# Optimization experiments

Hardware: AMD Instinct MI355X
Metric: run time of the kernel (lower is better)

## Reference

```python
import jax, jax.numpy as jnp
import numpy as np

# BCQLinear packed forward: weight[o, i] reconstructed from per-(out,group,bit)
# alpha scales and +/-1 binary codes via einsum('oib,oiab->oia'), then a plain
# out-channel-wise matmul (in_ch_wise=False) plus bias. beta is NOT used in the
# packed forward path of the original module.

B, S = 2, 1024          # token dims (m...)
O = 4096                 # out_features
G, A, NB = 32, 128, 3    # n_groups, group_size, n_bits; in_features = G*A = 4096


def setup_inputs() -> dict:
    key = jax.random.key(0)
    k1, k2, k3, k4 = jax.random.split(key, 4)
    x = jax.random.normal(k1, (B, S, G * A), dtype=jnp.float32)
    # binary codes are strictly +/-1 (Packer.unpack yields sign bits)
    b = jnp.sign(jax.random.normal(k2, (O, G, A, NB)))
    binary = jnp.where(b == 0, 1.0, b).astype(jnp.float32)
    # alpha scales are small positive magnitudes in practice
    alpha = jax.random.uniform(k3, (O, G, NB), dtype=jnp.float32,
                               minval=0.01, maxval=0.1)
    bias = 0.01 * jax.random.normal(k4, (O,), dtype=jnp.float32)
    return {"input": x, "binary": binary, "alpha": alpha, "bias": bias}


def reference(input, binary, alpha, bias):
    # dequantize: [O, G, A] -> [O, I]
    weight = jnp.einsum('oib,oiab->oia', alpha, binary).reshape(binary.shape[0], -1)
    # out-channel-wise matmul: m...i, oi -> m...o
    out = jnp.einsum('msi,oi->mso', input, weight) + bias
    return out
```

## Files before the change

### kernel.cpp

```cpp
#include <hip/hip_runtime.h>
#include <hip/hip_bf16.h>
#include <stdint.h>

typedef __bf16 bf16x8 __attribute__((ext_vector_type(8)));
typedef __bf16 bf16x4 __attribute__((ext_vector_type(4)));
typedef float  f32x4  __attribute__((ext_vector_type(4)));

static constexpr int Mdim = 2048;
static constexpr int Ndim = 4096;
static constexpr int Kdim = 4096;
static constexpr int DQ_BLOCKS = (Ndim * Kdim / 4) / 256;
static constexpr int CVT_BLOCKS = (Mdim * Kdim / 8) / 256;

__global__ __launch_bounds__(256)
void prep(const float* __restrict__ binary, const float* __restrict__ alpha,
          const float* __restrict__ x, __bf16* __restrict__ w,
          __bf16* __restrict__ xb) {
  const int b = blockIdx.x;
  if (b < DQ_BLOCKS) {
    long e = ((long)b * 256 + threadIdx.x) * 4;
    int o = (int)(e >> 12);
    int i = (int)(e & 4095);
    int g = i >> 7;
    const float* al = alpha + ((long)o * 32 + g) * 3;
    float a0 = al[0], a1 = al[1], a2 = al[2];
    const float4* bs = (const float4*)(binary + e * 3);
    float4 b0 = bs[0], b1 = bs[1], b2 = bs[2];
    bf16x4 wv;
    wv[0] = (__bf16)(a0 * b0.x + a1 * b0.y + a2 * b0.z);
    wv[1] = (__bf16)(a0 * b0.w + a1 * b1.x + a2 * b1.y);
    wv[2] = (__bf16)(a0 * b1.z + a1 * b1.w + a2 * b2.x);
    wv[3] = (__bf16)(a0 * b2.y + a1 * b2.z + a2 * b2.w);
    *(bf16x4*)(w + e) = wv;
  } else {
    long e = ((long)(b - DQ_BLOCKS) * 256 + threadIdx.x) * 8;
    float4 v0 = *(const float4*)(x + e);
    float4 v1 = *(const float4*)(x + e + 4);
    bf16x8 r;
    r[0] = (__bf16)v0.x; r[1] = (__bf16)v0.y; r[2] = (__bf16)v0.z; r[3] = (__bf16)v0.w;
    r[4] = (__bf16)v1.x; r[5] = (__bf16)v1.y; r[6] = (__bf16)v1.z; r[7] = (__bf16)v1.w;
    *(bf16x8*)(xb + e) = r;
  }
}

__global__ __launch_bounds__(256)
void reduce_add(const __bf16* __restrict__ p, const float* __restrict__ bias,
                float* __restrict__ out) {
  long e = ((long)blockIdx.x * 256 + threadIdx.x) * 8;
  bf16x8 a = *(const bf16x8*)(p + e);
  bf16x8 c = *(const bf16x8*)(p + (long)Mdim * Ndim + e);
  int col = (int)(e & (Ndim - 1));
  float4 bv0 = *(const float4*)(bias + col);
  float4 bv1 = *(const float4*)(bias + col + 4);
  float4 r0, r1;
  r0.x = (float)a[0] + (float)c[0] + bv0.x;
  r0.y = (float)a[1] + (float)c[1] + bv0.y;
  r0.z = (float)a[2] + (float)c[2] + bv0.z;
  r0.w = (float)a[3] + (float)c[3] + bv0.w;
  r1.x = (float)a[4] + (float)c[4] + bv1.x;
  r1.y = (float)a[5] + (float)c[5] + bv1.y;
  r1.z = (float)a[6] + (float)c[6] + bv1.z;
  r1.w = (float)a[7] + (float)c[7] + bv1.w;
  *(float4*)(out + e) = r0;
  *(float4*)(out + e + 4) = r1;
}

static constexpr int BK = 64;
static constexpr int KSLICE = 2048;
static constexpr int NT = KSLICE / BK;
static constexpr int ITERS = NT / 2;

__device__ __forceinline__ void g2l16(const void* g, void* l) {
  __builtin_amdgcn_global_load_lds(
      (const __attribute__((address_space(1))) void*)g,
      (__attribute__((address_space(3))) void*)l, 16, 0, 0);
}

#define BAR()    __builtin_amdgcn_s_barrier()
#define LGKM0()  asm volatile("s_waitcnt lgkmcnt(0)" ::: "memory")
#define SCHED0() __builtin_amdgcn_sched_barrier(0)

#define STAGE_A(t, H, b) do { \
  _Pragma("unroll") for (int j_ = 0; j_ < 2; ++j_) \
    g2l16(baseA[j_] + (H) * 128 * Kdim + (t) * 64, \
          sm + (b) * 65536 + (H) * 16384 + (w * 2 + j_) * 1024); \
} while (0)
#define STAGE_B(t, H, b) do { \
  _Pragma("unroll") for (int j_ = 0; j_ < 2; ++j_) \
    g2l16(baseB[j_] + (H) * 128 * Kdim + (t) * 64, \
          sm + (b) * 65536 + 32768 + (H) * 16384 + (w * 2 + j_) * 1024); \
} while (0)

#define LOAD_A4(dst, b, m0_) do { \
  _Pragma("unroll") for (int m_ = 0; m_ < 4; ++m_) \
    _Pragma("unroll") for (int h_ = 0; h_ < 2; ++h_) \
      dst[m_][h_] = *(const bf16x8*)(sm + (b) * 65536 + aoffbase + ((m0_) + m_) * 2048 + swz[h_]); \
} while (0)
#define LOAD_B2(dst, b, n0_) do { \
  _Pragma("unroll") for (int n_ = 0; n_ < 2; ++n_) \
    _Pragma("unroll") for (int h_ = 0; h_ < 2; ++h_) \
      dst[n_][h_] = *(const bf16x8*)(sm + (b) * 65536 + boffbase + ((n0_) + n_) * 2048 + swz[h_]); \
} while (0)

#define MMA8(fa_, fb_, m0_, n0_) do { \
  __builtin_amdgcn_s_setprio(1); \
  _Pragma("unroll") for (int m_ = 0; m_ < 4; ++m_) \
    _Pragma("unroll") for (int n_ = 0; n_ < 2; ++n_) { \
      acc[(m0_) + m_][(n0_) + n_] = __builtin_amdgcn_mfma_f32_16x16x32_bf16( \
          fa_[m_][0], fb_[n_][0], acc[(m0_) + m_][(n0_) + n_], 0, 0, 0); \
      acc[(m0_) + m_][(n0_) + n_] = __builtin_amdgcn_mfma_f32_16x16x32_bf16( \
          fa_[m_][1], fb_[n_][1], acc[(m0_) + m_][(n0_) + n_], 0, 0, 0); \
    } \
  __builtin_amdgcn_s_setprio(0); \
} while (0)

__global__ __launch_bounds__(512, 2)
void gemm8(const __bf16* __restrict__ A, const __bf16* __restrict__ Bw,
           __bf16* __restrict__ P) {
  __shared__ __align__(128) char sm[131072];
  const int tid = threadIdx.x, lane = tid & 63, w = tid >> 6;
  const int wm = w >> 2, wn = w & 3;

  const int bid = blockIdx.x;
  const int logical = (bid & 7) * 32 + (bid >> 3);
  const int ks = logical >> 7;
  const int tile = logical & 127;
  const int tm = tile & 7, tn = tile >> 3;
  const int kbase = ks * KSLICE;

  __bf16* Pout = P + (long)ks * Mdim * Ndim;

  const int rlo = lane >> 3;
  const int gsw = (lane & 7) ^ rlo;
  const __bf16* baseA[2];
  const __bf16* baseB[2];
#pragma unroll
  for (int j = 0; j < 2; ++j) {
    int rp = (w * 2 + j) * 8 + rlo;
    baseA[j] = A  + (long)(tm * 256 + rp) * Kdim + kbase + gsw * 8;
    baseB[j] = Bw + (long)(tn * 256 + rp) * Kdim + kbase + gsw * 8;
  }

  int swz[2];
#pragma unroll
  for (int h = 0; h < 2; ++h)
    swz[h] = (((h * 4 + (lane >> 4)) ^ (lane & 7)) << 4);
  const int aoffbase = (wm * 128 + (lane & 15)) * 128;
  const int boffbase = 32768 + (wn * 64 + (lane & 15)) * 128;

  f32x4 acc[8][4] = {};

  STAGE_A(0, 0, 0); STAGE_A(0, 1, 0); STAGE_B(0, 0, 0); STAGE_B(0, 1, 0);
  STAGE_B(1, 0, 1); STAGE_B(1, 1, 1);
  asm volatile("s_waitcnt vmcnt(4)" ::: "memory");
  BAR();

  bf16x8 fa[4][2], fb01[2][2], fb23[2][2];

  for (int i = 0; i < ITERS; ++i) {
    const int t0 = 2 * i, t1 = 2 * i + 1;
    const bool pf = (i < ITERS - 1);
    LOAD_A4(fa, 0, 0); LOAD_B2(fb01, 0, 0);
    STAGE_A(t1, 0, 1);
    BAR(); LGKM0(); SCHED0();
    MMA8(fa, fb01, 0, 0);
    BAR();
    LOAD_B2(fb23, 0, 2);
    STAGE_A(t1, 1, 1);
    BAR(); LGKM0(); SCHED0();
    MMA8(fa, fb23, 0, 2);
    BAR();
    LOAD_A4(fa, 0, 4);
    if (pf) STAGE_B(t0 + 2, 0, 0);
    BAR(); LGKM0(); SCHED0();
    MMA8(fa, fb01, 4, 0);
    BAR();
    if (pf) STAGE_B(t0 + 2, 1, 0);
    if (i == ITERS - 1) { asm volatile("s_waitcnt vmcnt(0)" ::: "memory"); }
    else                { asm volatile("s_waitcnt vmcnt(4)" ::: "memory"); }
    BAR();
    MMA8(fa, fb23, 4, 2);
    BAR();
    LOAD_A4(fa, 1, 0); LOAD_B2(fb01, 1, 0);
    if (pf) STAGE_A(t0 + 2, 0, 0);
    BAR(); LGKM0(); SCHED0();
    MMA8(fa, fb01, 0, 0);
    BAR();
    LOAD_B2(fb23, 1, 2);
    if (pf) STAGE_A(t0 + 2, 1, 0);
    BAR(); LGKM0(); SCHED0();
    MMA8(fa, fb23, 0, 2);
    BAR();
    LOAD_A4(fa, 1, 4);
    if (pf) STAGE_B(t1 + 2, 0, 1);
    BAR(); LGKM0(); SCHED0();
    MMA8(fa, fb01, 4, 0);
    BAR();
    if (pf) STAGE_B(t1 + 2, 1, 1);
    asm volatile("s_waitcnt vmcnt(4)" ::: "memory");
    BAR();
    MMA8(fa, fb23, 4, 2);
    BAR();
  }

  const int r4 = (lane >> 4) * 4;
  const int cl = lane & 15;
#pragma unroll
  for (int m = 0; m < 8; ++m)
#pragma unroll
    for (int n = 0; n < 4; ++n)
#pragma unroll
      for (int r = 0; r < 4; ++r) {
        int row = tm * 256 + wm * 128 + m * 16 + r4 + r;
        int col = tn * 256 + wn * 64 + n * 16 + cl;
        Pout[(long)row * Ndim + col] = (__bf16)acc[m][n][r];
      }
}

extern "C" void kernel_launch(void* const* d_in, const int* in_sizes, int n_in,
                              void* d_out, int out_size, void* d_ws, size_t ws_size,
                              hipStream_t stream) {
  const float* x      = (const float*)d_in[0];
  const float* binary = (const float*)d_in[1];
  const float* alpha  = (const float*)d_in[2];
  const float* bias   = (const float*)d_in[3];
  float* out = (float*)d_out;

  __bf16* wb = (__bf16*)d_ws;
  __bf16* xb = wb + (size_t)Ndim * Kdim;
  __bf16* pp = xb + (size_t)Mdim * Kdim;

  prep<<<dim3(DQ_BLOCKS + CVT_BLOCKS), 256, 0, stream>>>(binary, alpha, x, wb, xb);
  gemm8<<<dim3(256), 512, 0, stream>>>(xb, wb, pp);
  reduce_add<<<dim3(Mdim * Ndim / 8 / 256), 256, 0, stream>>>(pp, bias, out);
}
```

Baseline: 123.3 us.

## Replace split-K GEMM and reduce kernel with full-K 256x128 tiles and fused bias

Drops the split-K decomposition and its separate reduce_add kernel. Each of the 256 blocks now computes a 256x128 output tile over the full K range and writes fp32 output with the bias added directly. It switches to a three-stage LDS ring buffer (48KB per stage) with a deeper prefetch distance. This removes the bf16 partial-sum round trip and one kernel launch, and avoids the rounding of partials to bf16. In exchange, each block runs twice as many K iterations and the tile has a lower compute-to-load ratio, so B is reloaded more often.

```diff
diff --git a/kernel.cpp b/kernel.cpp
--- a/kernel.cpp
+++ b/kernel.cpp
@@ -43,32 +43,8 @@
   }
 }
 
-__global__ __launch_bounds__(256)
-void reduce_add(const __bf16* __restrict__ p, const float* __restrict__ bias,
-                float* __restrict__ out) {
-  long e = ((long)blockIdx.x * 256 + threadIdx.x) * 8;
-  bf16x8 a = *(const bf16x8*)(p + e);
-  bf16x8 c = *(const bf16x8*)(p + (long)Mdim * Ndim + e);
-  int col = (int)(e & (Ndim - 1));
-  float4 bv0 = *(const float4*)(bias + col);
-  float4 bv1 = *(const float4*)(bias + col + 4);
-  float4 r0, r1;
-  r0.x = (float)a[0] + (float)c[0] + bv0.x;
-  r0.y = (float)a[1] + (float)c[1] + bv0.y;
-  r0.z = (float)a[2] + (float)c[2] + bv0.z;
-  r0.w = (float)a[3] + (float)c[3] + bv0.w;
-  r1.x = (float)a[4] + (float)c[4] + bv1.x;
-  r1.y = (float)a[5] + (float)c[5] + bv1.y;
-  r1.z = (float)a[6] + (float)c[6] + bv1.z;
-  r1.w = (float)a[7] + (float)c[7] + bv1.w;
-  *(float4*)(out + e) = r0;
-  *(float4*)(out + e + 4) = r1;
-}
-
-static constexpr int BK = 64;
-static constexpr int KSLICE = 2048;
-static constexpr int NT = KSLICE / BK;
-static constexpr int ITERS = NT / 2;
+static constexpr int NT = Kdim / 64;
+static constexpr int BUF = 49152;
 
 __device__ __forceinline__ void g2l16(const void* g, void* l) {
   __builtin_amdgcn_global_load_lds(
@@ -79,56 +55,54 @@
 #define BAR()    __builtin_amdgcn_s_barrier()
 #define LGKM0()  asm volatile("s_waitcnt lgkmcnt(0)" ::: "memory")
 #define SCHED0() __builtin_amdgcn_sched_barrier(0)
+#define VMC6()   asm volatile("s_waitcnt vmcnt(6)" ::: "memory")
+#define VMC0()   asm volatile("s_waitcnt vmcnt(0)" ::: "memory")
 
-#define STAGE_A(t, H, b) do { \
+#define STAGE_A(t, H, bo) do { \
   _Pragma("unroll") for (int j_ = 0; j_ < 2; ++j_) \
-    g2l16(baseA[j_] + (H) * 128 * Kdim + (t) * 64, \
-          sm + (b) * 65536 + (H) * 16384 + (w * 2 + j_) * 1024); \
+    g2l16(baseA[j_] + (H) * 128 * (long)Kdim + (t) * 64, \
+          sm + (bo) + (H) * 16384 + (w * 2 + j_) * 1024); \
 } while (0)
-#define STAGE_B(t, H, b) do { \
+#define STAGE_B(t, bo) do { \
   _Pragma("unroll") for (int j_ = 0; j_ < 2; ++j_) \
-    g2l16(baseB[j_] + (H) * 128 * Kdim + (t) * 64, \
-          sm + (b) * 65536 + 32768 + (H) * 16384 + (w * 2 + j_) * 1024); \
+    g2l16(baseB[j_] + (t) * 64, \
+          sm + (bo) + 32768 + (w * 2 + j_) * 1024); \
 } while (0)
 
-#define LOAD_A4(dst, b, m0_) do { \
+#define LOAD_A4(dst, bo, m0_) do { \
   _Pragma("unroll") for (int m_ = 0; m_ < 4; ++m_) \
     _Pragma("unroll") for (int h_ = 0; h_ < 2; ++h_) \
-      dst[m_][h_] = *(const bf16x8*)(sm + (b) * 65536 + aoffbase + ((m0_) + m_) * 2048 + swz[h_]); \
+      dst[m_][h_] = *(const bf16x8*)(sm + (bo) + aoffbase + ((m0_) + m_) * 2048 + swz[h_]); \
 } while (0)
-#define LOAD_B2(dst, b, n0_) do { \
+#define LOAD_B2(dst, bo) do { \
   _Pragma("unroll") for (int n_ = 0; n_ < 2; ++n_) \
     _Pragma("unroll") for (int h_ = 0; h_ < 2; ++h_) \
-      dst[n_][h_] = *(const bf16x8*)(sm + (b) * 65536 + boffbase + ((n0_) + n_) * 2048 + swz[h_]); \
+      dst[n_][h_] = *(const bf16x8*)(sm + (bo) + boffbase + n_ * 2048 + swz[h_]); \
 } while (0)
 
-#define MMA8(fa_, fb_, m0_, n0_) do { \
+#define MMA16(fa_, fb_, m0_) do { \
   __builtin_amdgcn_s_setprio(1); \
   _Pragma("unroll") for (int m_ = 0; m_ < 4; ++m_) \
     _Pragma("unroll") for (int n_ = 0; n_ < 2; ++n_) { \
-      acc[(m0_) + m_][(n0_) + n_] = __builtin_amdgcn_mfma_f32_16x16x32_bf16( \
-          fa_[m_][0], fb_[n_][0], acc[(m0_) + m_][(n0_) + n_], 0, 0, 0); \
-      acc[(m0_) + m_][(n0_) + n_] = __builtin_amdgcn_mfma_f32_16x16x32_bf16( \
-          fa_[m_][1], fb_[n_][1], acc[(m0_) + m_][(n0_) + n_], 0, 0, 0); \
+      acc[(m0_) + m_][n_] = __builtin_amdgcn_mfma_f32_16x16x32_bf16( \
+          fa_[m_][0], fb_[n_][0], acc[(m0_) + m_][n_], 0, 0, 0); \
+      acc[(m0_) + m_][n_] = __builtin_amdgcn_mfma_f32_16x16x32_bf16( \
+          fa_[m_][1], fb_[n_][1], acc[(m0_) + m_][n_], 0, 0, 0); \
     } \
   __builtin_amdgcn_s_setprio(0); \
 } while (0)
 
 __global__ __launch_bounds__(512, 2)
-void gemm8(const __bf16* __restrict__ A, const __bf16* __restrict__ Bw,
-           __bf16* __restrict__ P) {
-  __shared__ __align__(128) char sm[131072];
+void gemm3(const __bf16* __restrict__ A, const __bf16* __restrict__ Bw,
+           const float* __restrict__ bias, float* __restrict__ out) {
+  __shared__ __align__(128) char sm[3 * BUF];
   const int tid = threadIdx.x, lane = tid & 63, w = tid >> 6;
   const int wm = w >> 2, wn = w & 3;
 
   const int bid = blockIdx.x;
   const int logical = (bid & 7) * 32 + (bid >> 3);
-  const int ks = logical >> 7;
-  const int tile = logical & 127;
-  const int tm = tile & 7, tn = tile >> 3;
-  const int kbase = ks * KSLICE;
-
-  __bf16* Pout = P + (long)ks * Mdim * Ndim;
+  const int tm = logical & 7;
+  const int tn = logical >> 3;
 
   const int rlo = lane >> 3;
   const int gsw = (lane & 7) ^ rlo;
@@ -137,8 +111,8 @@
 #pragma unroll
   for (int j = 0; j < 2; ++j) {
     int rp = (w * 2 + j) * 8 + rlo;
-    baseA[j] = A  + (long)(tm * 256 + rp) * Kdim + kbase + gsw * 8;
-    baseB[j] = Bw + (long)(tn * 256 + rp) * Kdim + kbase + gsw * 8;
+    baseA[j] = A  + (long)(tm * 256 + rp) * Kdim + gsw * 8;
+    baseB[j] = Bw + (long)(tn * 128 + rp) * Kdim + gsw * 8;
   }
 
   int swz[2];
@@ -146,75 +120,49 @@
   for (int h = 0; h < 2; ++h)
     swz[h] = (((h * 4 + (lane >> 4)) ^ (lane & 7)) << 4);
   const int aoffbase = (wm * 128 + (lane & 15)) * 128;
-  const int boffbase = 32768 + (wn * 64 + (lane & 15)) * 128;
+  const int boffbase = 32768 + (wn * 32 + (lane & 15)) * 128;
 
-  f32x4 acc[8][4] = {};
+  f32x4 acc[8][2] = {};
 
-  STAGE_A(0, 0, 0); STAGE_A(0, 1, 0); STAGE_B(0, 0, 0); STAGE_B(0, 1, 0);
-  STAGE_B(1, 0, 1); STAGE_B(1, 1, 1);
-  asm volatile("s_waitcnt vmcnt(4)" ::: "memory");
+  STAGE_A(0, 0, 0);     STAGE_A(0, 1, 0);     STAGE_B(0, 0);
+  STAGE_A(1, 0, BUF);   STAGE_A(1, 1, BUF);   STAGE_B(1, BUF);
+  VMC6();
   BAR();
 
-  bf16x8 fa[4][2], fb01[2][2], fb23[2][2];
+  bf16x8 fa[4][2], fa2[4][2], fb[2][2];
+  int ba = 0, bb = BUF, bc = 2 * BUF;
 
-  for (int i = 0; i < ITERS; ++i) {
-    const int t0 = 2 * i, t1 = 2 * i + 1;
-    const bool pf = (i < ITERS - 1);
-    LOAD_A4(fa, 0, 0); LOAD_B2(fb01, 0, 0);
-    STAGE_A(t1, 0, 1);
+  for (int t = 0; t < NT; ++t) {
+    const bool pf = (t + 2 < NT);
+    LOAD_A4(fa, ba, 0);
+    LOAD_B2(fb, ba);
+    if (pf) STAGE_A(t + 2, 0, bc);
     BAR(); LGKM0(); SCHED0();
-    MMA8(fa, fb01, 0, 0);
+    MMA16(fa, fb, 0);
     BAR();
-    LOAD_B2(fb23, 0, 2);
-    STAGE_A(t1, 1, 1);
+    LOAD_A4(fa2, ba, 4);
+    if (pf) { STAGE_A(t + 2, 1, bc); STAGE_B(t + 2, bc); }
+    if (t < NT - 2) { VMC6(); } else { VMC0(); }
     BAR(); LGKM0(); SCHED0();
-    MMA8(fa, fb23, 0, 2);
+    MMA16(fa2, fb, 4);
     BAR();
-    LOAD_A4(fa, 0, 4);
-    if (pf) STAGE_B(t0 + 2, 0, 0);
-    BAR(); LGKM0(); SCHED0();
-    MMA8(fa, fb01, 4, 0);
-    BAR();
-    if (pf) STAGE_B(t0 + 2, 1, 0);
-    if (i == ITERS - 1) { asm volatile("s_waitcnt vmcnt(0)" ::: "memory"); }
-    else                { asm volatile("s_waitcnt vmcnt(4)" ::: "memory"); }
-    BAR();
-    MMA8(fa, fb23, 4, 2);
-    BAR();
-    LOAD_A4(fa, 1, 0); LOAD_B2(fb01, 1, 0);
-    if (pf) STAGE_A(t0 + 2, 0, 0);
-    BAR(); LGKM0(); SCHED0();
-    MMA8(fa, fb01, 0, 0);
-    BAR();
-    LOAD_B2(fb23, 1, 2);
-    if (pf) STAGE_A(t0 + 2, 1, 0);
-    BAR(); LGKM0(); SCHED0();
-    MMA8(fa, fb23, 0, 2);
-    BAR();
-    LOAD_A4(fa, 1, 4);
-    if (pf) STAGE_B(t1 + 2, 0, 1);
-    BAR(); LGKM0(); SCHED0();
-    MMA8(fa, fb01, 4, 0);
-    BAR();
-    if (pf) STAGE_B(t1 + 2, 1, 1);
-    asm volatile("s_waitcnt vmcnt(4)" ::: "memory");
-    BAR();
-    MMA8(fa, fb23, 4, 2);
-    BAR();
+    int tmp = ba; ba = bb; bb = bc; bc = tmp;
   }
 
   const int r4 = (lane >> 4) * 4;
   const int cl = lane & 15;
 #pragma unroll
-  for (int m = 0; m < 8; ++m)
+  for (int n = 0; n < 2; ++n) {
+    const int col = tn * 128 + wn * 32 + n * 16 + cl;
+    const float bv = bias[col];
 #pragma unroll
-    for (int n = 0; n < 4; ++n)
+    for (int m = 0; m < 8; ++m)
 #pragma unroll
       for (int r = 0; r < 4; ++r) {
-        int row = tm * 256 + wm * 128 + m * 16 + r4 + r;
-        int col = tn * 256 + wn * 64 + n * 16 + cl;
-        Pout[(long)row * Ndim + col] = (__bf16)acc[m][n][r];
+        const int row = tm * 256 + wm * 128 + m * 16 + r4 + r;
+        out[(long)row * Ndim + col] = acc[m][n][r] + bv;
       }
+  }
 }
 
 extern "C" void kernel_launch(void* const* d_in, const int* in_sizes, int n_in,
@@ -228,9 +176,7 @@
 
   __bf16* wb = (__bf16*)d_ws;
   __bf16* xb = wb + (size_t)Ndim * Kdim;
-  __bf16* pp = xb + (size_t)Mdim * Kdim;
 
   prep<<<dim3(DQ_BLOCKS + CVT_BLOCKS), 256, 0, stream>>>(binary, alpha, x, wb, xb);
-  gemm8<<<dim3(256), 512, 0, stream>>>(xb, wb, pp);
-  reduce_add<<<dim3(Mdim * Ndim / 8 / 256), 256, 0, stream>>>(pp, bias, out);
+  gemm3<<<dim3(256), 512, 0, stream>>>(xb, wb, bias, out);
 }
```

After: 122.8 us. About the same (-0.5%).

## Restructure GEMM K-loop prefetch into per-buffer partial stages and widen dequant

Applied to the files above, without the earlier changes.

The GEMM main loop is rebuilt as a KTILE macro. Each k-tile refills its own LDS buffer for tile t+2 in four pieces, each issued right after the fragments it overwrites have been read into registers. The prologue now stages two full tiles, and a vmcnt(8) gate replaces the old interleaved A/B staging across buffers. The aim is to keep more global-to-LDS traffic in flight and overlap it with MFMA work. The dequant prep kernel also handles 8 weights per thread with a 16-byte bf16 store instead of 4 weights per thread, which cuts thread count and widens memory transactions. The risk is that the fine-grained reuse of the same buffer depends on the row-to-piece mapping and wait counts being exactly right.

```diff
diff --git a/kernel.cpp b/kernel.cpp
--- a/kernel.cpp
+++ b/kernel.cpp
@@ -3,13 +3,12 @@
 #include <stdint.h>
 
 typedef __bf16 bf16x8 __attribute__((ext_vector_type(8)));
-typedef __bf16 bf16x4 __attribute__((ext_vector_type(4)));
 typedef float  f32x4  __attribute__((ext_vector_type(4)));
 
 static constexpr int Mdim = 2048;
 static constexpr int Ndim = 4096;
 static constexpr int Kdim = 4096;
-static constexpr int DQ_BLOCKS = (Ndim * Kdim / 4) / 256;
+static constexpr int DQ_BLOCKS = (Ndim * Kdim / 8) / 256;
 static constexpr int CVT_BLOCKS = (Mdim * Kdim / 8) / 256;
 
 __global__ __launch_bounds__(256)
@@ -18,20 +17,23 @@
           __bf16* __restrict__ xb) {
   const int b = blockIdx.x;
   if (b < DQ_BLOCKS) {
-    long e = ((long)b * 256 + threadIdx.x) * 4;
+    long e = ((long)b * 256 + threadIdx.x) * 8;
     int o = (int)(e >> 12);
-    int i = (int)(e & 4095);
-    int g = i >> 7;
+    int g = (int)((e & 4095) >> 7);
     const float* al = alpha + ((long)o * 32 + g) * 3;
     float a0 = al[0], a1 = al[1], a2 = al[2];
-    const float4* bs = (const float4*)(binary + e * 3);
-    float4 b0 = bs[0], b1 = bs[1], b2 = bs[2];
-    bf16x4 wv;
-    wv[0] = (__bf16)(a0 * b0.x + a1 * b0.y + a2 * b0.z);
-    wv[1] = (__bf16)(a0 * b0.w + a1 * b1.x + a2 * b1.y);
-    wv[2] = (__bf16)(a0 * b1.z + a1 * b1.w + a2 * b2.x);
-    wv[3] = (__bf16)(a0 * b2.y + a1 * b2.z + a2 * b2.w);
-    *(bf16x4*)(w + e) = wv;
+    const float4* q = (const float4*)(binary + e * 3);
+    float4 q0 = q[0], q1 = q[1], q2 = q[2], q3 = q[3], q4 = q[4], q5 = q[5];
+    bf16x8 wv;
+    wv[0] = (__bf16)(a0 * q0.x + a1 * q0.y + a2 * q0.z);
+    wv[1] = (__bf16)(a0 * q0.w + a1 * q1.x + a2 * q1.y);
+    wv[2] = (__bf16)(a0 * q1.z + a1 * q1.w + a2 * q2.x);
+    wv[3] = (__bf16)(a0 * q2.y + a1 * q2.z + a2 * q2.w);
+    wv[4] = (__bf16)(a0 * q3.x + a1 * q3.y + a2 * q3.z);
+    wv[5] = (__bf16)(a0 * q3.w + a1 * q4.x + a2 * q4.y);
+    wv[6] = (__bf16)(a0 * q4.z + a1 * q4.w + a2 * q5.x);
+    wv[7] = (__bf16)(a0 * q5.y + a1 * q5.z + a2 * q5.w);
+    *(bf16x8*)(w + e) = wv;
   } else {
     long e = ((long)(b - DQ_BLOCKS) * 256 + threadIdx.x) * 8;
     float4 v0 = *(const float4*)(x + e);
@@ -65,10 +67,9 @@
   *(float4*)(out + e + 4) = r1;
 }
 
-static constexpr int BK = 64;
 static constexpr int KSLICE = 2048;
-static constexpr int NT = KSLICE / BK;
-static constexpr int ITERS = NT / 2;
+static constexpr int NT = KSLICE / 64;
+static constexpr int HB = 65536;
 
 __device__ __forceinline__ void g2l16(const void* g, void* l) {
   __builtin_amdgcn_global_load_lds(
@@ -79,27 +80,35 @@
 #define BAR()    __builtin_amdgcn_s_barrier()
 #define LGKM0()  asm volatile("s_waitcnt lgkmcnt(0)" ::: "memory")
 #define SCHED0() __builtin_amdgcn_sched_barrier(0)
-
-#define STAGE_A(t, H, b) do { \
-  _Pragma("unroll") for (int j_ = 0; j_ < 2; ++j_) \
-    g2l16(baseA[j_] + (H) * 128 * Kdim + (t) * 64, \
-          sm + (b) * 65536 + (H) * 16384 + (w * 2 + j_) * 1024); \
-} while (0)
-#define STAGE_B(t, H, b) do { \
-  _Pragma("unroll") for (int j_ = 0; j_ < 2; ++j_) \
-    g2l16(baseB[j_] + (H) * 128 * Kdim + (t) * 64, \
-          sm + (b) * 65536 + 32768 + (H) * 16384 + (w * 2 + j_) * 1024); \
-} while (0)
-
-#define LOAD_A4(dst, b, m0_) do { \
+#define GATE8()  asm volatile("s_waitcnt vmcnt(8)" ::: "memory")
+#define GATE0()  asm volatile("s_waitcnt vmcnt(0)" ::: "memory")
+
+#define STAGE_A1(t, bo) do { \
+  g2l16(baseA +                 (long)(t) * 64, sm + (bo) +     0 + w * 1024); \
+  g2l16(baseA + 128L * Kdim   + (long)(t) * 64, sm + (bo) + 16384 + w * 1024); \
+} while (0)
+#define STAGE_A2(t, bo) do { \
+  g2l16(baseA +  64L * Kdim   + (long)(t) * 64, sm + (bo) +  8192 + w * 1024); \
+  g2l16(baseA + 192L * Kdim   + (long)(t) * 64, sm + (bo) + 24576 + w * 1024); \
+} while (0)
+#define STAGE_B1(t, bo) do { \
+  g2l16(baseB +                 (long)(t) * 64, sm + (bo) + 32768 + bq * 1024); \
+  g2l16(baseB +   8L * Kdim   + (long)(t) * 64, sm + (bo) + 32768 + bq * 1024 + 1024); \
+} while (0)
+#define STAGE_B2(t, bo) do { \
+  g2l16(baseB +  32L * Kdim   + (long)(t) * 64, sm + (bo) + 32768 + bq * 1024 + 4096); \
+  g2l16(baseB +  40L * Kdim   + (long)(t) * 64, sm + (bo) + 32768 + bq * 1024 + 5120); \
+} while (0)
+
+#define LOAD_A4(dst, bo, m0_) do { \
   _Pragma("unroll") for (int m_ = 0; m_ < 4; ++m_) \
     _Pragma("unroll") for (int h_ = 0; h_ < 2; ++h_) \
-      dst[m_][h_] = *(const bf16x8*)(sm + (b) * 65536 + aoffbase + ((m0_) + m_) * 2048 + swz[h_]); \
-} while (0)
-#define LOAD_B2(dst, b, n0_) do { \
+      dst[m_][h_] = *(const bf16x8*)(sm + (bo) + aoffbase + ((m0_) + m_) * 2048 + swz[h_]); \
+} while (0)
+#define LOAD_B2(dst, bo, n0_) do { \
   _Pragma("unroll") for (int n_ = 0; n_ < 2; ++n_) \
     _Pragma("unroll") for (int h_ = 0; h_ < 2; ++h_) \
-      dst[n_][h_] = *(const bf16x8*)(sm + (b) * 65536 + boffbase + ((n0_) + n_) * 2048 + swz[h_]); \
+      dst[n_][h_] = *(const bf16x8*)(sm + (bo) + boffbase + ((n0_) + n_) * 2048 + swz[h_]); \
 } while (0)
 
 #define MMA8(fa_, fb_, m0_, n0_) do { \
@@ -114,10 +123,35 @@
   __builtin_amdgcn_s_setprio(0); \
 } while (0)
 
+#define KTILE(t_, bo, PF_, LASTGATE) do { \
+   \
+  LOAD_A4(fa, bo, 0); LOAD_B2(fb01, bo, 0); \
+  BAR(); LGKM0(); SCHED0(); \
+  MMA8(fa, fb01, 0, 0); \
+  BAR(); \
+   \
+  LOAD_B2(fb23, bo, 2); \
+  if (PF_) { STAGE_A1((t_) + 2, bo); STAGE_B1((t_) + 2, bo); } \
+  BAR(); LGKM0(); SCHED0(); \
+  MMA8(fa, fb23, 0, 2); \
+  BAR(); \
+   \
+  LOAD_A4(fa, bo, 4); \
+  if (PF_) STAGE_B2((t_) + 2, bo); \
+  BAR(); LGKM0(); SCHED0(); \
+  MMA8(fa, fb01, 4, 0); \
+  BAR(); \
+   \
+  if (PF_) { STAGE_A2((t_) + 2, bo); GATE8(); } else { LASTGATE; } \
+  BAR(); \
+  MMA8(fa, fb23, 4, 2); \
+  BAR(); \
+} while (0)
+
 __global__ __launch_bounds__(512, 2)
-void gemm8(const __bf16* __restrict__ A, const __bf16* __restrict__ Bw,
-           __bf16* __restrict__ P) {
-  __shared__ __align__(128) char sm[131072];
+void gemm256(const __bf16* __restrict__ A, const __bf16* __restrict__ Bw,
+             __bf16* __restrict__ P) {
+  __shared__ __align__(128) char sm[2 * HB];
   const int tid = threadIdx.x, lane = tid & 63, w = tid >> 6;
   const int wm = w >> 2, wn = w & 3;
 
@@ -132,14 +166,10 @@
 
   const int rlo = lane >> 3;
   const int gsw = (lane & 7) ^ rlo;
-  const __bf16* baseA[2];
-  const __bf16* baseB[2];
-#pragma unroll
-  for (int j = 0; j < 2; ++j) {
-    int rp = (w * 2 + j) * 8 + rlo;
-    baseA[j] = A  + (long)(tm * 256 + rp) * Kdim + kbase + gsw * 8;
-    baseB[j] = Bw + (long)(tn * 256 + rp) * Kdim + kbase + gsw * 8;
-  }
+  const __bf16* baseA = A + (long)(tm * 256 + w * 8 + rlo) * Kdim + kbase + gsw * 8;
+  const __bf16* baseB = Bw + (long)(tn * 256 + (w >> 1) * 64 + (w & 1) * 16 + rlo) * Kdim
+                        + kbase + gsw * 8;
+  const int bq = (w >> 1) * 8 + (w & 1) * 2;
 
   int swz[2];
 #pragma unroll
@@ -149,58 +179,18 @@
   const int boffbase = 32768 + (wn * 64 + (lane & 15)) * 128;
 
   f32x4 acc[8][4] = {};
-
-  STAGE_A(0, 0, 0); STAGE_A(0, 1, 0); STAGE_B(0, 0, 0); STAGE_B(0, 1, 0);
-  STAGE_B(1, 0, 1); STAGE_B(1, 1, 1);
-  asm volatile("s_waitcnt vmcnt(4)" ::: "memory");
+  bf16x8 fa[4][2], fb01[2][2], fb23[2][2];
+
+  STAGE_A1(0, 0);  STAGE_B1(0, 0);  STAGE_B2(0, 0);  STAGE_A2(0, 0);
+  STAGE_A1(1, HB); STAGE_B1(1, HB); STAGE_B2(1, HB); STAGE_A2(1, HB);
+  GATE8();
   BAR();
 
-  bf16x8 fa[4][2], fb01[2][2], fb23[2][2];
-
-  for (int i = 0; i < ITERS; ++i) {
+  for (int i = 0; i < NT / 2; ++i) {
     const int t0 = 2 * i, t1 = 2 * i + 1;
-    const bool pf = (i < ITERS - 1);
-    LOAD_A4(fa, 0, 0); LOAD_B2(fb01, 0, 0);
-    STAGE_A(t1, 0, 1);
-    BAR(); LGKM0(); SCHED0();
-    MMA8(fa, fb01, 0, 0);
-    BAR();
-    LOAD_B2(fb23, 0, 2);
-    STAGE_A(t1, 1, 1);
-    BAR(); LGKM0(); SCHED0();
-    MMA8(fa, fb23, 0, 2);
-    BAR();
-    LOAD_A4(fa, 0, 4);
-    if (pf) STAGE_B(t0 + 2, 0, 0);
-    BAR(); LGKM0(); SCHED0();
-    MMA8(fa, fb01, 4, 0);
-    BAR();
-    if (pf) STAGE_B(t0 + 2, 1, 0);
-    if (i == ITERS - 1) { asm volatile("s_waitcnt vmcnt(0)" ::: "memory"); }
-    else                { asm volatile("s_waitcnt vmcnt(4)" ::: "memory"); }
-    BAR();
-    MMA8(fa, fb23, 4, 2);
-    BAR();
-    LOAD_A4(fa, 1, 0); LOAD_B2(fb01, 1, 0);
-    if (pf) STAGE_A(t0 + 2, 0, 0);
-    BAR(); LGKM0(); SCHED0();
-    MMA8(fa, fb01, 0, 0);
-    BAR();
-    LOAD_B2(fb23, 1, 2);
-    if (pf) STAGE_A(t0 + 2, 1, 0);
-    BAR(); LGKM0(); SCHED0();
-    MMA8(fa, fb23, 0, 2);
-    BAR();
-    LOAD_A4(fa, 1, 4);
-    if (pf) STAGE_B(t1 + 2, 0, 1);
-    BAR(); LGKM0(); SCHED0();
-    MMA8(fa, fb01, 4, 0);
-    BAR();
-    if (pf) STAGE_B(t1 + 2, 1, 1);
-    asm volatile("s_waitcnt vmcnt(4)" ::: "memory");
-    BAR();
-    MMA8(fa, fb23, 4, 2);
-    BAR();
+    const bool pf = (i < NT / 2 - 1);
+    KTILE(t0, 0,  pf, GATE0());
+    KTILE(t1, HB, pf, GATE0());
   }
 
   const int r4 = (lane >> 4) * 4;
@@ -231,6 +221,6 @@
   __bf16* pp = xb + (size_t)Mdim * Kdim;
 
   prep<<<dim3(DQ_BLOCKS + CVT_BLOCKS), 256, 0, stream>>>(binary, alpha, x, wb, xb);
-  gemm8<<<dim3(256), 512, 0, stream>>>(xb, wb, pp);
+  gemm256<<<dim3(256), 512, 0, stream>>>(xb, wb, pp);
   reduce_add<<<dim3(Mdim * Ndim / 8 / 256), 256, 0, stream>>>(pp, bias, out);
 }
```

Result: no change. 123.3 us (-0.1%).
